# Optimization experiments

Hardware: AMD Instinct MI355X
Metric: run time of the kernel (lower is better)

Reference implementation:

```python
import jax, jax.numpy as jnp
import numpy as np


def setup_inputs() -> dict:
    key = jax.random.key(0)
    k_h, k_src, k_dst, k_w = jax.random.split(key, 4)
    N, F, E, OUT = 100000, 128, 640000, 16
    h = jax.random.normal(k_h, (N, F), dtype=jnp.float32)
    src = jax.random.randint(k_src, (E,), 0, N, dtype=jnp.int64)
    dst = jax.random.randint(k_dst, (E,), 0, N, dtype=jnp.int64)
    # Linear(2F, OUT): weight [OUT, 2F], bias [OUT]
    W = jax.random.normal(k_w, (OUT, 2 * F), dtype=jnp.float32) / np.sqrt(2.0 * F)
    b = jnp.zeros((OUT,), dtype=jnp.float32)
    return {"h": h, "src": src, "dst": dst, "W": W, "b": b}


def reference(h, src, dst, W, b):
    # Per-edge gather of source/dest node features, concat, linear.
    # Dropout is identity in eval mode (p=0.2 during training only).
    h_u = h[src]                      # [E, F]
    h_v = h[dst]                      # [E, F]
    F_dim = h.shape[1]
    W_u, W_v = W[:, :F_dim], W[:, F_dim:]
    # Equivalent to concat([h_u, h_v], -1) @ W.T + b, without materializing concat
    score = jnp.einsum('ef,of->eo', h_u, W_u) + jnp.einsum('ef,of->eo', h_v, W_v) + b
    return score
```

## Files before the change

### kernel.cpp

```cpp
#include <hip/hip_runtime.h>
#include <hip/hip_bf16.h>

#define F_DIM 128
#define OUT_DIM 16

__global__ __launch_bounds__(256) void proj_kernel(
    const float* __restrict__ h, const float* __restrict__ W,
    const float* __restrict__ b, float* __restrict__ P, int N)
{
    __shared__ float Ws[16 * 256];
    {
        const float4* W4 = (const float4*)W;
        float4* Ws4 = (float4*)Ws;
        #pragma unroll
        for (int i = 0; i < 4; ++i)
            Ws4[threadIdx.x + i * 256] = W4[threadIdx.x + i * 256];
    }
    __syncthreads();

    const int half = threadIdx.x >> 7;
    const int row  = blockIdx.x * 128 + (threadIdx.x & 127);
    if (row >= N) return;

    const float4* hr = (const float4*)(h + (size_t)row * F_DIM);
    const float* Wbase = Ws + half * 128;

    float acc[16];
    #pragma unroll
    for (int o = 0; o < 16; ++o) acc[o] = 0.0f;

    #pragma unroll 4
    for (int k4 = 0; k4 < 32; ++k4) {
        float4 hv = hr[k4];
        #pragma unroll
        for (int o = 0; o < 16; ++o) {
            const float4 wv = *(const float4*)(Wbase + o * 256 + k4 * 4);
            acc[o] = fmaf(hv.x, wv.x, acc[o]);
            acc[o] = fmaf(hv.y, wv.y, acc[o]);
            acc[o] = fmaf(hv.z, wv.z, acc[o]);
            acc[o] = fmaf(hv.w, wv.w, acc[o]);
        }
    }

    if (half == 0) {
        #pragma unroll
        for (int o = 0; o < 16; ++o) acc[o] += b[o];
    }

    float4* Pq = (float4*)(P + (size_t)row * 32 + half * 16);
    Pq[0] = make_float4(acc[0],  acc[1],  acc[2],  acc[3]);
    Pq[1] = make_float4(acc[4],  acc[5],  acc[6],  acc[7]);
    Pq[2] = make_float4(acc[8],  acc[9],  acc[10], acc[11]);
    Pq[3] = make_float4(acc[12], acc[13], acc[14], acc[15]);
}

__global__ __launch_bounds__(256) void gather_kernel(
    const float* __restrict__ P, const int* __restrict__ src,
    const int* __restrict__ dst, float* __restrict__ out, int E)
{
    const int tid = blockIdx.x * blockDim.x + threadIdx.x;
    const int e = tid >> 2;
    const int q = tid & 3;
    if (e >= E) return;
    const int s = src[e];
    const int d = dst[e];
    float4 pu = *(const float4*)(P + (size_t)s * 32 + q * 4);
    float4 pv = *(const float4*)(P + (size_t)d * 32 + 16 + q * 4);
    float4 r;
    r.x = pu.x + pv.x;
    r.y = pu.y + pv.y;
    r.z = pu.z + pv.z;
    r.w = pu.w + pv.w;
    ((float4*)out)[tid] = r;
}

__global__ __launch_bounds__(256) void direct_kernel(
    const float* __restrict__ h, const int* __restrict__ src,
    const int* __restrict__ dst, const float* __restrict__ W,
    const float* __restrict__ b, float* __restrict__ out, int E)
{
    const int tid = blockIdx.x * blockDim.x + threadIdx.x;
    if (tid >= E * OUT_DIM) return;
    const int e = tid >> 4;
    const int o = tid & 15;
    const float* hu = h + (size_t)src[e] * F_DIM;
    const float* hv = h + (size_t)dst[e] * F_DIM;
    const float* wu = W + (size_t)o * 256;
    const float* wv = wu + 128;
    float acc = b[o];
    for (int k = 0; k < 128; ++k) acc = fmaf(hu[k], wu[k], acc);
    for (int k = 0; k < 128; ++k) acc = fmaf(hv[k], wv[k], acc);
    out[tid] = acc;
}

extern "C" void kernel_launch(void* const* d_in, const int* in_sizes, int n_in,
                              void* d_out, int out_size, void* d_ws, size_t ws_size,
                              hipStream_t stream) {
    const float* h   = (const float*)d_in[0];
    const int*   src = (const int*)d_in[1];
    const int*   dst = (const int*)d_in[2];
    const float* W   = (const float*)d_in[3];
    const float* b   = (const float*)d_in[4];
    float* out = (float*)d_out;

    const int N = in_sizes[0] / F_DIM;
    const int E = in_sizes[1];

    const size_t p_bytes = (size_t)N * 32 * sizeof(float);

    if (ws_size >= p_bytes) {
        float* P = (float*)d_ws;
        const int blocks1 = (N + 127) / 128;
        proj_kernel<<<blocks1, 256, 0, stream>>>(h, W, b, P, N);
        const int total2 = E * 4;
        const int blocks2 = (total2 + 255) / 256;
        gather_kernel<<<blocks2, 256, 0, stream>>>(P, src, dst, out, E);
    } else {
        const int total = E * OUT_DIM;
        const int blocks = (total + 255) / 256;
        direct_kernel<<<blocks, 256, 0, stream>>>(h, src, dst, W, b, out, E);
    }
}
```

Measured before the change: 142.0 us.

## Stage h tiles in swizzled LDS and read transposed W via uniform loads

A small kernel now transposes W into a [k][32] layout in workspace, so the projection kernel can read weights with wave-uniform addresses (scalar loads) instead of from LDS. The h rows for each block are loaded into LDS with coalesced float4 loads and an XOR swizzle, in two 64-column chunks. Previously each thread read its own row directly, which was strided and uncoalesced. This adds an extra kernel launch, block barriers, and the need for the workspace to also hold Wt.

```diff
diff --git a/kernel.cpp b/kernel.cpp
--- a/kernel.cpp
+++ b/kernel.cpp
@@ -4,54 +4,76 @@
 #define F_DIM 128
 #define OUT_DIM 16
 
+__global__ __launch_bounds__(256) void wtrans_kernel(
+    const float* __restrict__ W, float* __restrict__ Wt)
+{
+    int tid = blockIdx.x * 256 + threadIdx.x;
+    if (tid >= 128 * 32) return;
+    int k   = tid >> 5;
+    int j   = tid & 31;
+    int o   = j & 15;
+    int sel = j >> 4;
+    Wt[tid] = W[o * 256 + sel * 128 + k];
+}
+
 __global__ __launch_bounds__(256) void proj_kernel(
-    const float* __restrict__ h, const float* __restrict__ W,
+    const float* __restrict__ h, const float* __restrict__ Wt,
     const float* __restrict__ b, float* __restrict__ P, int N)
 {
-    __shared__ float Ws[16 * 256];
-    {
-        const float4* W4 = (const float4*)W;
-        float4* Ws4 = (float4*)Ws;
-        #pragma unroll
-        for (int i = 0; i < 4; ++i)
-            Ws4[threadIdx.x + i * 256] = W4[threadIdx.x + i * 256];
-    }
-    __syncthreads();
+    __shared__ float hs[128 * 64];
 
-    const int half = threadIdx.x >> 7;
-    const int row  = blockIdx.x * 128 + (threadIdx.x & 127);
-    if (row >= N) return;
-
-    const float4* hr = (const float4*)(h + (size_t)row * F_DIM);
-    const float* Wbase = Ws + half * 128;
+    const int t    = threadIdx.x;
+    const int half = __builtin_amdgcn_readfirstlane(t >> 7);
+    const int r    = t & 127;
+    const int row0 = blockIdx.x * 128;
 
     float acc[16];
     #pragma unroll
     for (int o = 0; o < 16; ++o) acc[o] = 0.0f;
 
-    #pragma unroll 4
-    for (int k4 = 0; k4 < 32; ++k4) {
-        float4 hv = hr[k4];
+    for (int ck = 0; ck < 2; ++ck) {
+        const int kbase = ck * 64;
         #pragma unroll
-        for (int o = 0; o < 16; ++o) {
-            const float4 wv = *(const float4*)(Wbase + o * 256 + k4 * 4);
-            acc[o] = fmaf(hv.x, wv.x, acc[o]);
-            acc[o] = fmaf(hv.y, wv.y, acc[o]);
-            acc[o] = fmaf(hv.z, wv.z, acc[o]);
-            acc[o] = fmaf(hv.w, wv.w, acc[o]);
+        for (int i = 0; i < 8; ++i) {
+            int f  = i * 256 + t;
+            int sr = f >> 4;
+            int k4 = f & 15;
+            int g  = row0 + sr;
+            if (g >= N) g = N - 1;
+            const float4 v = *(const float4*)(h + (size_t)g * F_DIM + kbase + k4 * 4);
+            int c = k4 ^ (sr & 7);
+            *(float4*)(hs + sr * 64 + c * 4) = v;
         }
+        __syncthreads();
+
+        #pragma unroll 4
+        for (int K4 = 0; K4 < 16; ++K4) {
+            int c = K4 ^ (r & 7);
+            const float4 hv = *(const float4*)(hs + r * 64 + c * 4);
+            const float* wrow = Wt + (size_t)(kbase + K4 * 4) * 32 + half * 16;
+            #pragma unroll
+            for (int j = 0; j < 4; ++j) {
+                const float hk = (&hv.x)[j];
+                #pragma unroll
+                for (int o = 0; o < 16; ++o)
+                    acc[o] = fmaf(wrow[j * 32 + o], hk, acc[o]);
+            }
+        }
+        __syncthreads();
     }
 
-    if (half == 0) {
-        #pragma unroll
-        for (int o = 0; o < 16; ++o) acc[o] += b[o];
+    const int grow = row0 + r;
+    if (grow < N) {
+        if (half == 0) {
+            #pragma unroll
+            for (int o = 0; o < 16; ++o) acc[o] += b[o];
+        }
+        float4* Pq = (float4*)(P + (size_t)grow * 32 + half * 16);
+        Pq[0] = make_float4(acc[0],  acc[1],  acc[2],  acc[3]);
+        Pq[1] = make_float4(acc[4],  acc[5],  acc[6],  acc[7]);
+        Pq[2] = make_float4(acc[8],  acc[9],  acc[10], acc[11]);
+        Pq[3] = make_float4(acc[12], acc[13], acc[14], acc[15]);
     }
-
-    float4* Pq = (float4*)(P + (size_t)row * 32 + half * 16);
-    Pq[0] = make_float4(acc[0],  acc[1],  acc[2],  acc[3]);
-    Pq[1] = make_float4(acc[4],  acc[5],  acc[6],  acc[7]);
-    Pq[2] = make_float4(acc[8],  acc[9],  acc[10], acc[11]);
-    Pq[3] = make_float4(acc[12], acc[13], acc[14], acc[15]);
 }
 
 __global__ __launch_bounds__(256) void gather_kernel(
@@ -106,17 +128,24 @@
     const int N = in_sizes[0] / F_DIM;
     const int E = in_sizes[1];
 
-    const size_t p_bytes = (size_t)N * 32 * sizeof(float);
+    const size_t p_bytes  = (size_t)N * 32 * sizeof(float);
+    const size_t p_al     = (p_bytes + 255) & ~(size_t)255;
+    const size_t wt_bytes = 128 * 32 * sizeof(float);
 
-    if (ws_size >= p_bytes) {
-        float* P = (float*)d_ws;
+    if (ws_size >= p_al + wt_bytes) {
+        float* P  = (float*)d_ws;
+        float* Wt = (float*)((char*)d_ws + p_al);
+
+        wtrans_kernel<<<16, 256, 0, stream>>>(W, Wt);
+
         const int blocks1 = (N + 127) / 128;
-        proj_kernel<<<blocks1, 256, 0, stream>>>(h, W, b, P, N);
-        const int total2 = E * 4;
+        proj_kernel<<<blocks1, 256, 0, stream>>>(h, Wt, b, P, N);
+
+        const int total2  = E * 4;
         const int blocks2 = (total2 + 255) / 256;
         gather_kernel<<<blocks2, 256, 0, stream>>>(P, src, dst, out, E);
     } else {
-        const int total = E * OUT_DIM;
+        const int total  = E * OUT_DIM;
         const int blocks = (total + 255) / 256;
         direct_kernel<<<blocks, 256, 0, stream>>>(h, src, dst, W, b, out, E);
     }
```

Result: faster. 138.6 us (-2.4%).

## Compute node projection with split-fp16 MFMA and use nontemporal gather stores

Applied to the files above, without the earlier changes.

Replaces the scalar FMA node-projection kernel with an MFMA 16x16x32 f16 kernel. To keep near-fp32 accuracy, both h and W are split into hi/lo fp16 parts and three MFMA products are accumulated. A small prep kernel lays out W in the MFMA B-operand order inside the workspace. The gather kernel now writes its output with nontemporal stores. This adds an extra launch and some approximation error from the fp16 split, in exchange for cheaper projection compute.

```diff
diff --git a/kernel.cpp b/kernel.cpp
--- a/kernel.cpp
+++ b/kernel.cpp
@@ -4,54 +4,84 @@
 #define F_DIM 128
 #define OUT_DIM 16
 
-__global__ __launch_bounds__(256) void proj_kernel(
-    const float* __restrict__ h, const float* __restrict__ W,
-    const float* __restrict__ b, float* __restrict__ P, int N)
+typedef _Float16 half8 __attribute__((ext_vector_type(8)));
+typedef float floatx4 __attribute__((ext_vector_type(4)));
+
+__global__ __launch_bounds__(256) void wprep_kernel(
+    const float* __restrict__ W, _Float16* __restrict__ Bhi,
+    _Float16* __restrict__ Blo)
 {
-    __shared__ float Ws[16 * 256];
-    {
-        const float4* W4 = (const float4*)W;
-        float4* Ws4 = (float4*)Ws;
+    int tid = blockIdx.x * 256 + threadIdx.x;
+    if (tid >= 4096) return;
+    int j    = tid & 7;
+    int lane = (tid >> 3) & 63;
+    int t    = (tid >> 9) & 1;
+    int s    = (tid >> 10) & 3;
+    int n = lane & 15;
+    int q = lane >> 4;
+    int k = s * 32 + q * 8 + j;
+    float w = W[n * 256 + t * 128 + k];
+    _Float16 hi = (_Float16)w;
+    _Float16 lo = (_Float16)(w - (float)hi);
+    Bhi[tid] = hi;
+    Blo[tid] = lo;
+}
+
+__global__ __launch_bounds__(256) void proj_mfma_kernel(
+    const float* __restrict__ h, const _Float16* __restrict__ Bhi,
+    const _Float16* __restrict__ Blo, const float* __restrict__ b,
+    float* __restrict__ P, int N)
+{
+    const int lane = threadIdx.x & 63;
+    const int wave = threadIdx.x >> 6;
+    const int n = lane & 15;
+    const int q = lane >> 4;
+    const int row_base = blockIdx.x * 64 + wave * 16;
+    if (row_base >= N) return;
+
+    int arow = row_base + n;
+    if (arow >= N) arow = N - 1;
+    const float* hrow = h + (size_t)arow * F_DIM + q * 8;
+
+    floatx4 c0 = {0.f, 0.f, 0.f, 0.f};
+    floatx4 c1 = {0.f, 0.f, 0.f, 0.f};
+
+    #pragma unroll
+    for (int s = 0; s < 4; ++s) {
+        float av[8];
+        *(float4*)(av)     = *(const float4*)(hrow + s * 32);
+        *(float4*)(av + 4) = *(const float4*)(hrow + s * 32 + 4);
+        half8 ah, al;
         #pragma unroll
-        for (int i = 0; i < 4; ++i)
-            Ws4[threadIdx.x + i * 256] = W4[threadIdx.x + i * 256];
+        for (int j = 0; j < 8; ++j) {
+            _Float16 hi = (_Float16)av[j];
+            ah[j] = hi;
+            al[j] = (_Float16)(av[j] - (float)hi);
+        }
+        const int base0 = (s * 2 + 0) * 512 + lane * 8;
+        const int base1 = (s * 2 + 1) * 512 + lane * 8;
+        half8 bh0 = *(const half8*)(Bhi + base0);
+        half8 bl0 = *(const half8*)(Blo + base0);
+        half8 bh1 = *(const half8*)(Bhi + base1);
+        half8 bl1 = *(const half8*)(Blo + base1);
+
+        c0 = __builtin_amdgcn_mfma_f32_16x16x32_f16(ah, bh0, c0, 0, 0, 0);
+        c0 = __builtin_amdgcn_mfma_f32_16x16x32_f16(ah, bl0, c0, 0, 0, 0);
+        c0 = __builtin_amdgcn_mfma_f32_16x16x32_f16(al, bh0, c0, 0, 0, 0);
+        c1 = __builtin_amdgcn_mfma_f32_16x16x32_f16(ah, bh1, c1, 0, 0, 0);
+        c1 = __builtin_amdgcn_mfma_f32_16x16x32_f16(ah, bl1, c1, 0, 0, 0);
+        c1 = __builtin_amdgcn_mfma_f32_16x16x32_f16(al, bh1, c1, 0, 0, 0);
     }
-    __syncthreads();
 
-    const int half = threadIdx.x >> 7;
-    const int row  = blockIdx.x * 128 + (threadIdx.x & 127);
-    if (row >= N) return;
-
-    const float4* hr = (const float4*)(h + (size_t)row * F_DIM);
-    const float* Wbase = Ws + half * 128;
-
-    float acc[16];
+    const float bn = b[n];
     #pragma unroll
-    for (int o = 0; o < 16; ++o) acc[o] = 0.0f;
-
-    #pragma unroll 4
-    for (int k4 = 0; k4 < 32; ++k4) {
-        float4 hv = hr[k4];
-        #pragma unroll
-        for (int o = 0; o < 16; ++o) {
-            const float4 wv = *(const float4*)(Wbase + o * 256 + k4 * 4);
-            acc[o] = fmaf(hv.x, wv.x, acc[o]);
-            acc[o] = fmaf(hv.y, wv.y, acc[o]);
-            acc[o] = fmaf(hv.z, wv.z, acc[o]);
-            acc[o] = fmaf(hv.w, wv.w, acc[o]);
+    for (int reg = 0; reg < 4; ++reg) {
+        int row = row_base + q * 4 + reg;
+        if (row < N) {
+            P[(size_t)row * 32 + n]      = c0[reg] + bn;
+            P[(size_t)row * 32 + 16 + n] = c1[reg];
         }
     }
-
-    if (half == 0) {
-        #pragma unroll
-        for (int o = 0; o < 16; ++o) acc[o] += b[o];
-    }
-
-    float4* Pq = (float4*)(P + (size_t)row * 32 + half * 16);
-    Pq[0] = make_float4(acc[0],  acc[1],  acc[2],  acc[3]);
-    Pq[1] = make_float4(acc[4],  acc[5],  acc[6],  acc[7]);
-    Pq[2] = make_float4(acc[8],  acc[9],  acc[10], acc[11]);
-    Pq[3] = make_float4(acc[12], acc[13], acc[14], acc[15]);
 }
 
 __global__ __launch_bounds__(256) void gather_kernel(
@@ -64,14 +94,10 @@
     if (e >= E) return;
     const int s = src[e];
     const int d = dst[e];
-    float4 pu = *(const float4*)(P + (size_t)s * 32 + q * 4);
-    float4 pv = *(const float4*)(P + (size_t)d * 32 + 16 + q * 4);
-    float4 r;
-    r.x = pu.x + pv.x;
-    r.y = pu.y + pv.y;
-    r.z = pu.z + pv.z;
-    r.w = pu.w + pv.w;
-    ((float4*)out)[tid] = r;
+    const floatx4 pu = *(const floatx4*)(P + (size_t)s * 32 + q * 4);
+    const floatx4 pv = *(const floatx4*)(P + (size_t)d * 32 + 16 + q * 4);
+    const floatx4 r = pu + pv;
+    __builtin_nontemporal_store(r, (floatx4*)out + tid);
 }
 
 __global__ __launch_bounds__(256) void direct_kernel(
@@ -106,17 +132,25 @@
     const int N = in_sizes[0] / F_DIM;
     const int E = in_sizes[1];
 
-    const size_t p_bytes = (size_t)N * 32 * sizeof(float);
+    const size_t p_bytes  = (size_t)N * 32 * sizeof(float);
+    const size_t p_al     = (p_bytes + 255) & ~(size_t)255;
+    const size_t bf_bytes = 4096 * sizeof(_Float16);
 
-    if (ws_size >= p_bytes) {
-        float* P = (float*)d_ws;
-        const int blocks1 = (N + 127) / 128;
-        proj_kernel<<<blocks1, 256, 0, stream>>>(h, W, b, P, N);
-        const int total2 = E * 4;
+    if (ws_size >= p_al + 2 * bf_bytes) {
+        float*    P   = (float*)d_ws;
+        _Float16* Bhi = (_Float16*)((char*)d_ws + p_al);
+        _Float16* Blo = Bhi + 4096;
+
+        wprep_kernel<<<16, 256, 0, stream>>>(W, Bhi, Blo);
+
+        const int blocks1 = (N + 63) / 64;
+        proj_mfma_kernel<<<blocks1, 256, 0, stream>>>(h, Bhi, Blo, b, P, N);
+
+        const int total2  = E * 4;
         const int blocks2 = (total2 + 255) / 256;
         gather_kernel<<<blocks2, 256, 0, stream>>>(P, src, dst, out, E);
     } else {
-        const int total = E * OUT_DIM;
+        const int total  = E * OUT_DIM;
         const int blocks = (total + 255) / 256;
         direct_kernel<<<blocks, 256, 0, stream>>>(h, src, dst, W, b, out, E);
     }
```

Result: faster. 131.7 us (-7.3%).
